# Optimization experiments

Hardware: AMD Instinct MI355X
Metric: run time of the kernel (lower is better)

The kernel has to match this reference:

```python
import jax, jax.numpy as jnp
import numpy as np

N = 100000       # nodes
E = 3200000      # edges
DIN = 128        # input_dim
H = 64           # hidden_dim
DEMB = 32        # embedding_dim
G = 256          # num graphs


def setup_inputs() -> dict:
    key = jax.random.key(0)
    ks = jax.random.split(key, 10)
    x = jax.random.normal(ks[0], (N, DIN), dtype=jnp.float32)
    edge_index = jax.random.randint(ks[1], (2, E), 0, N, dtype=jnp.int64)
    batch = jnp.sort(jax.random.randint(ks[2], (N,), 0, G, dtype=jnp.int64))
    W1 = jax.random.normal(ks[3], (DIN, H), dtype=jnp.float32) * (1.0 / np.sqrt(DIN))
    b1 = jnp.zeros((H,), dtype=jnp.float32)
    W2 = jax.random.normal(ks[4], (H, H), dtype=jnp.float32) * (1.0 / np.sqrt(H))
    b2 = jnp.zeros((H,), dtype=jnp.float32)
    Wl = jax.random.normal(ks[5], (H, DEMB), dtype=jnp.float32) * (1.0 / np.sqrt(H))
    bl = jnp.zeros((DEMB,), dtype=jnp.float32)
    return {"x": x, "edge_index": edge_index, "batch": batch, "num_graphs": G,
            "W1": W1, "b1": b1, "W2": W2, "b2": b2, "Wl": Wl, "bl": bl}


def _gcn_conv(h, src, dst, W, b, n_nodes):
    # PyG GCNConv: add self-loops, symmetric D^{-1/2}(A+I)D^{-1/2} normalization,
    # linear transform first, then propagate.
    h = h @ W                                                  # [N, out]
    deg = jax.ops.segment_sum(jnp.ones((src.shape[0],), h.dtype), dst,
                              num_segments=n_nodes) + 1.0      # +1 self-loop
    dinv = jax.lax.rsqrt(deg)                                  # [N]
    coef = dinv[src] * dinv[dst]                               # [E]
    msgs = h[src] * coef[:, None]                              # [E, out]
    agg = jax.ops.segment_sum(msgs, dst, num_segments=n_nodes)
    agg = agg + h * (dinv * dinv)[:, None]                     # self-loop message
    return agg + b


def reference(x, edge_index, batch, num_graphs, W1, b1, W2, b2, Wl, bl):
    src, dst = edge_index[0], edge_index[1]
    n_nodes = x.shape[0]
    h = jax.nn.relu(_gcn_conv(x, src, dst, W1, b1, n_nodes))
    h = jax.nn.relu(_gcn_conv(h, src, dst, W2, b2, n_nodes))
    # global_mean_pool over batch ids
    sums = jax.ops.segment_sum(h, batch, num_segments=num_graphs)     # [G, H]
    counts = jax.ops.segment_sum(jnp.ones((n_nodes,), h.dtype), batch,
                                 num_segments=num_graphs)
    pooled = sums / jnp.maximum(counts, 1.0)[:, None]
    return pooled @ Wl + bl                                           # [G, DEMB]
```

## Files before the change

### kernel.cpp

```cpp
#include <hip/hip_runtime.h>

#define NN 100000
#define NE 3200000
#define DIN 128
#define HD 64
#define DEMB 32
#define NG 256
#define NBUCK ((NN + 255) / 256)
#define NPB 512
#define CHUNK ((NE + NPB - 1) / NPB)
#define NM (NBUCK * NPB)
#define NMB ((NM + 1023) / 1024)

typedef unsigned short u16;
typedef unsigned int u32;

__device__ __forceinline__ float bflo(u32 u) { return __uint_as_float(u << 16); }
__device__ __forceinline__ float bfhi(u32 u) { return __uint_as_float(u & 0xffff0000u); }
__device__ __forceinline__ u16 f2bf(float f) {
    u32 u = __float_as_uint(f);
    return (u16)((u + 0x7fffu + ((u >> 16) & 1u)) >> 16);
}

__global__ __launch_bounds__(256) void k_blkhist(const int* __restrict__ dst,
                                                 int* __restrict__ HM, int E) {
    __shared__ int h[NBUCK];
    int blk = blockIdx.x, t = threadIdx.x;
    for (int i = t; i < NBUCK; i += 256) h[i] = 0;
    __syncthreads();
    int beg = blk * CHUNK, end = min(E, beg + CHUNK);
    for (int j = beg + t; j < end; j += 256) atomicAdd(&h[dst[j] >> 8], 1);
    __syncthreads();
    for (int i = t; i < NBUCK; i += 256) HM[i * NPB + blk] = h[i];
}

__global__ __launch_bounds__(1024) void k_scanA(int* __restrict__ HM,
                                                int* __restrict__ bsum, int n) {
    __shared__ int s[1024];
    int t = threadIdx.x;
    int idx = blockIdx.x * 1024 + t;
    int v = (idx < n) ? HM[idx] : 0;
    s[t] = v;
    __syncthreads();
    for (int off = 1; off < 1024; off <<= 1) {
        int add = (t >= off) ? s[t - off] : 0;
        __syncthreads();
        s[t] += add;
        __syncthreads();
    }
    if (idx < n) HM[idx] = s[t] - v;
    if (t == 1023) bsum[blockIdx.x] = s[t];
}

__global__ void k_scan2(const int* __restrict__ bsum, int* __restrict__ boff, int nb) {
    if (threadIdx.x == 0 && blockIdx.x == 0) {
        int acc = 0;
        for (int b = 0; b < nb; b++) { boff[b] = acc; acc += bsum[b]; }
        boff[nb] = acc;
    }
}

__global__ void k_scanC(int* __restrict__ HM, const int* __restrict__ boff, int n) {
    int idx = blockIdx.x * blockDim.x + threadIdx.x;
    if (idx < n) HM[idx] += boff[idx >> 10];
}

__global__ __launch_bounds__(256) void k_place(const int* __restrict__ src,
                                               const int* __restrict__ dst,
                                               const int* __restrict__ HM,
                                               int* __restrict__ part, int E) {
    __shared__ int cur[NBUCK];
    int blk = blockIdx.x, t = threadIdx.x;
    for (int i = t; i < NBUCK; i += 256) cur[i] = HM[i * NPB + blk];
    __syncthreads();
    int beg = blk * CHUNK, end = min(E, beg + CHUNK);
    for (int j = beg + t; j < end; j += 256) {
        int d = dst[j], s = src[j];
        int pos = atomicAdd(&cur[d >> 8], 1);
        part[pos] = s | ((d & 255) << 17);
    }
}

__global__ __launch_bounds__(256) void k_phaseB(const int* __restrict__ part,
                                                const int* __restrict__ HM,
                                                int* __restrict__ rowptr,
                                                int* __restrict__ ssrc,
                                                float* __restrict__ dinv, int E) {
    __shared__ int cnt[256];
    __shared__ int sc[256];
    int b = blockIdx.x;
    int t = threadIdx.x;
    int beg = HM[b * NPB];
    int end = (b == NBUCK - 1) ? E : HM[(b + 1) * NPB];
    int node0 = b << 8;
    int nnode = NN - node0 < 256 ? NN - node0 : 256;
    cnt[t] = 0;
    __syncthreads();
    for (int j = beg + t; j < end; j += 256) atomicAdd(&cnt[part[j] >> 17], 1);
    __syncthreads();
    int v = cnt[t];
    sc[t] = v;
    __syncthreads();
    for (int off = 1; off < 256; off <<= 1) {
        int add = (t >= off) ? sc[t - off] : 0;
        __syncthreads();
        sc[t] += add;
        __syncthreads();
    }
    int excl = sc[t] - v;
    if (t < nnode) {
        rowptr[node0 + t] = beg + excl;
        dinv[node0 + t] = rsqrtf((float)v + 1.0f);
    }
    if (b == NBUCK - 1 && t == 0) rowptr[NN] = E;
    __syncthreads();
    cnt[t] = beg + excl;
    __syncthreads();
    for (int j = beg + t; j < end; j += 256) {
        int e = part[j];
        int pos = atomicAdd(&cnt[e >> 17], 1);
        ssrc[pos] = e & 0x1FFFF;
    }
}

template <int K>
__global__ __launch_bounds__(256, 4) void k_gemm(const float* __restrict__ X,
                                                 const float* __restrict__ W,
                                                 const float* __restrict__ dinv,
                                                 u16* __restrict__ U, int n) {
    __shared__ __align__(16) float xt[32][68];
    __shared__ __align__(16) float wlc[32][64];
    int tid = threadIdx.x;
    int cg = tid & 15;
    int rs = tid >> 4;
    int row0 = blockIdx.x * 64;
    float4 acc0 = {0.f, 0.f, 0.f, 0.f};
    float4 acc1 = {0.f, 0.f, 0.f, 0.f};
    float4 acc2 = {0.f, 0.f, 0.f, 0.f};
    float4 acc3 = {0.f, 0.f, 0.f, 0.f};
    for (int kc = 0; kc < K; kc += 32) {
        __syncthreads();
        for (int p = 0; p < 2; ++p) {
            int idx = tid + p * 256;
            int r = idx >> 3;
            int c4 = idx & 7;
            int row = row0 + r;
            float4 v = {0.f, 0.f, 0.f, 0.f};
            if (row < n) v = *reinterpret_cast<const float4*>(&X[(size_t)row * K + kc + c4 * 4]);
            xt[c4 * 4 + 0][r] = v.x;
            xt[c4 * 4 + 1][r] = v.y;
            xt[c4 * 4 + 2][r] = v.z;
            xt[c4 * 4 + 3][r] = v.w;
        }
        for (int p = 0; p < 2; ++p) {
            int idx = tid + p * 256;
            int kr = idx >> 4;
            int c4 = idx & 15;
            *reinterpret_cast<float4*>(&wlc[kr][c4 * 4]) =
                *reinterpret_cast<const float4*>(&W[(size_t)(kc + kr) * 64 + c4 * 4]);
        }
        __syncthreads();
#pragma unroll
        for (int k = 0; k < 32; ++k) {
            float4 xv = *reinterpret_cast<const float4*>(&xt[k][rs * 4]);
            float4 wv = *reinterpret_cast<const float4*>(&wlc[k][cg * 4]);
            acc0.x += xv.x * wv.x; acc0.y += xv.x * wv.y; acc0.z += xv.x * wv.z; acc0.w += xv.x * wv.w;
            acc1.x += xv.y * wv.x; acc1.y += xv.y * wv.y; acc1.z += xv.y * wv.z; acc1.w += xv.y * wv.w;
            acc2.x += xv.z * wv.x; acc2.y += xv.z * wv.y; acc2.z += xv.z * wv.z; acc2.w += xv.z * wv.w;
            acc3.x += xv.w * wv.x; acc3.y += xv.w * wv.y; acc3.z += xv.w * wv.z; acc3.w += xv.w * wv.w;
        }
    }
    int rbase = row0 + rs * 4;
    float dv;
    if (rbase + 0 < n) { dv = dinv[rbase + 0];
        ushort4 o = {f2bf(acc0.x * dv), f2bf(acc0.y * dv), f2bf(acc0.z * dv), f2bf(acc0.w * dv)};
        *reinterpret_cast<ushort4*>(&U[(size_t)(rbase + 0) * 64 + cg * 4]) = o; }
    if (rbase + 1 < n) { dv = dinv[rbase + 1];
        ushort4 o = {f2bf(acc1.x * dv), f2bf(acc1.y * dv), f2bf(acc1.z * dv), f2bf(acc1.w * dv)};
        *reinterpret_cast<ushort4*>(&U[(size_t)(rbase + 1) * 64 + cg * 4]) = o; }
    if (rbase + 2 < n) { dv = dinv[rbase + 2];
        ushort4 o = {f2bf(acc2.x * dv), f2bf(acc2.y * dv), f2bf(acc2.z * dv), f2bf(acc2.w * dv)};
        *reinterpret_cast<ushort4*>(&U[(size_t)(rbase + 2) * 64 + cg * 4]) = o; }
    if (rbase + 3 < n) { dv = dinv[rbase + 3];
        ushort4 o = {f2bf(acc3.x * dv), f2bf(acc3.y * dv), f2bf(acc3.z * dv), f2bf(acc3.w * dv)};
        *reinterpret_cast<ushort4*>(&U[(size_t)(rbase + 3) * 64 + cg * 4]) = o; }
}

__global__ void k_gather(const int* __restrict__ rowptr, const int* __restrict__ ssrc,
                         const float* __restrict__ dinv, const u16* __restrict__ U,
                         const float* __restrict__ bias,
                         float* __restrict__ outbuf, int n) {
    int gtid = blockIdx.x * blockDim.x + threadIdx.x;
    int lane = gtid & 63;
    int g = lane & 7;
    int c = lane >> 3;
    int w = gtid >> 6;
    int nw = (gridDim.x * blockDim.x) >> 6;
    float bv = bias[lane];
    for (int d = w; d < n; d += nw) {
        int beg = rowptr[d], end = rowptr[d + 1];
        float4 aL0 = {0.f,0.f,0.f,0.f}, aH0 = {0.f,0.f,0.f,0.f};
        float4 aL1 = {0.f,0.f,0.f,0.f}, aH1 = {0.f,0.f,0.f,0.f};
        int j = beg;
        for (; j + 16 <= end; j += 16) {
            int s0 = ssrc[j + g];
            int s1 = ssrc[j + 8 + g];
            uint4 u0 = *reinterpret_cast<const uint4*>(&U[(size_t)s0 * 64 + c * 8]);
            uint4 u1 = *reinterpret_cast<const uint4*>(&U[(size_t)s1 * 64 + c * 8]);
            aL0.x += bflo(u0.x); aL0.y += bfhi(u0.x); aL0.z += bflo(u0.y); aL0.w += bfhi(u0.y);
            aH0.x += bflo(u0.z); aH0.y += bfhi(u0.z); aH0.z += bflo(u0.w); aH0.w += bfhi(u0.w);
            aL1.x += bflo(u1.x); aL1.y += bfhi(u1.x); aL1.z += bflo(u1.y); aL1.w += bfhi(u1.y);
            aH1.x += bflo(u1.z); aH1.y += bfhi(u1.z); aH1.z += bflo(u1.w); aH1.w += bfhi(u1.w);
        }
        if (j + 8 <= end) {
            int s0 = ssrc[j + g];
            uint4 u0 = *reinterpret_cast<const uint4*>(&U[(size_t)s0 * 64 + c * 8]);
            aL0.x += bflo(u0.x); aL0.y += bfhi(u0.x); aL0.z += bflo(u0.y); aL0.w += bfhi(u0.y);
            aH0.x += bflo(u0.z); aH0.y += bfhi(u0.z); aH0.z += bflo(u0.w); aH0.w += bfhi(u0.w);
            j += 8;
        }
        if (j + g < end) {
            int s1 = ssrc[j + g];
            uint4 u1 = *reinterpret_cast<const uint4*>(&U[(size_t)s1 * 64 + c * 8]);
            aL1.x += bflo(u1.x); aL1.y += bfhi(u1.x); aL1.z += bflo(u1.y); aL1.w += bfhi(u1.y);
            aH1.x += bflo(u1.z); aH1.y += bfhi(u1.z); aH1.z += bflo(u1.w); aH1.w += bfhi(u1.w);
        }
        aL0.x += aL1.x; aL0.y += aL1.y; aL0.z += aL1.z; aL0.w += aL1.w;
        aH0.x += aH1.x; aH0.y += aH1.y; aH0.z += aH1.z; aH0.w += aH1.w;
#pragma unroll
        for (int m = 1; m <= 4; m <<= 1) {
            aL0.x += __shfl_xor(aL0.x, m); aL0.y += __shfl_xor(aL0.y, m);
            aL0.z += __shfl_xor(aL0.z, m); aL0.w += __shfl_xor(aL0.w, m);
            aH0.x += __shfl_xor(aH0.x, m); aH0.y += __shfl_xor(aH0.y, m);
            aH0.z += __shfl_xor(aH0.z, m); aH0.w += __shfl_xor(aH0.w, m);
        }
        float4 q = (g & 4) ? aH0 : aL0;
        float hv = (g & 2) ? ((g & 1) ? q.w : q.z) : ((g & 1) ? q.y : q.x);
        float ud = bflo((u32)U[(size_t)d * 64 + lane] << 0) ;
        ud = __uint_as_float(((u32)U[(size_t)d * 64 + lane]) << 16);
        float dd = dinv[d];
        float h = (hv + ud) * dd + bv;
        h = h > 0.f ? h : 0.f;
        outbuf[(size_t)d * 64 + lane] = h;
    }
}

__global__ __launch_bounds__(256) void k_pool(const float* __restrict__ h,
                                              const int* __restrict__ batch,
                                              float* __restrict__ sums, int n) {
    int tid = blockIdx.x * blockDim.x + threadIdx.x;
    int wave = tid >> 6;
    int lane = tid & 63;
    int node0 = wave * 64;
    if (node0 >= n) return;
    int nodeEnd = min(n, node0 + 64);
    float acc = 0.f;
    int curg = batch[node0];
    for (int nd = node0; nd < nodeEnd; ++nd) {
        int g = batch[nd];
        if (g != curg) {
            atomicAdd(&sums[(size_t)curg * 64 + lane], acc);
            acc = 0.f;
            curg = g;
        }
        acc += h[(size_t)nd * 64 + lane];
    }
    atomicAdd(&sums[(size_t)curg * 64 + lane], acc);
}

__global__ void k_final(const float* __restrict__ sums, const int* __restrict__ batch,
                        const float* __restrict__ Wl, const float* __restrict__ bl,
                        float* __restrict__ out, int n) {
    __shared__ float pooled[64];
    int g = blockIdx.x;
    int t = threadIdx.x;
    int lo = 0, hi = n;
    while (lo < hi) { int m = (lo + hi) >> 1; if (batch[m] < g) lo = m + 1; else hi = m; }
    int lo2 = lo, hi2 = n;
    while (lo2 < hi2) { int m = (lo2 + hi2) >> 1; if (batch[m] < g + 1) lo2 = m + 1; else hi2 = m; }
    float c = (float)(lo2 - lo);
    c = c < 1.0f ? 1.0f : c;
    pooled[t] = sums[g * 64 + t] / c;
    __syncthreads();
    if (t < 32) {
        float acc = bl[t];
#pragma unroll 8
        for (int k = 0; k < 64; k++) acc += pooled[k] * Wl[k * 32 + t];
        out[g * 32 + t] = acc;
    }
}

extern "C" void kernel_launch(void* const* d_in, const int* in_sizes, int n_in,
                              void* d_out, int out_size, void* d_ws, size_t ws_size,
                              hipStream_t stream) {
    const float* x = (const float*)d_in[0];
    const int* ei = (const int*)d_in[1];
    const int* batch = (const int*)d_in[2];
    const float* W1 = (const float*)d_in[4];
    const float* b1 = (const float*)d_in[5];
    const float* W2 = (const float*)d_in[6];
    const float* b2 = (const float*)d_in[7];
    const float* Wl = (const float*)d_in[8];
    const float* bl = (const float*)d_in[9];
    float* out = (float*)d_out;

    const int* esrc = ei;
    const int* edst = ei + NE;

    char* ws = (char*)d_ws;
    size_t off = 0;
    auto alloc = [&](size_t bytes) {
        void* p = ws + off;
        off += (bytes + 255) & ~size_t(255);
        return p;
    };
    float* dinv   = (float*)alloc((size_t)NN * 4);
    int*   rowptr = (int*)alloc((size_t)(NN + 1) * 4);
    int*   HM     = (int*)alloc((size_t)NM * 4);
    int*   bsum   = (int*)alloc((size_t)(NMB + 1) * 4);
    int*   boff   = (int*)alloc((size_t)(NMB + 1) * 4);
    int*   ssrc   = (int*)alloc((size_t)NE * 4);
    u16*   tbuf   = (u16*)alloc((size_t)NE * 4);
    float* agg    = (float*)alloc((size_t)NN * HD * 4);
    float* sums   = (float*)alloc((size_t)NG * HD * 4);
    int* part = (int*)tbuf;

    k_blkhist<<<NPB, 256, 0, stream>>>(edst, HM, NE);
    k_scanA<<<NMB, 1024, 0, stream>>>(HM, bsum, NM);
    k_scan2<<<1, 64, 0, stream>>>(bsum, boff, NMB);
    k_scanC<<<(NM + 255) / 256, 256, 0, stream>>>(HM, boff, NM);
    k_place<<<NPB, 256, 0, stream>>>(esrc, edst, HM, part, NE);
    k_phaseB<<<NBUCK, 256, 0, stream>>>(part, HM, rowptr, ssrc, dinv, NE);

    k_gemm<DIN><<<(NN + 63) / 64, 256, 0, stream>>>(x, W1, dinv, tbuf, NN);
    k_gather<<<2048, 256, 0, stream>>>(rowptr, ssrc, dinv, tbuf, b1, agg, NN);

    k_gemm<HD><<<(NN + 63) / 64, 256, 0, stream>>>(agg, W2, dinv, tbuf, NN);
    k_gather<<<2048, 256, 0, stream>>>(rowptr, ssrc, dinv, tbuf, b2, agg, NN);

    hipMemsetAsync(sums, 0, (size_t)NG * HD * 4, stream);
    k_pool<<<(NN + 255) / 256, 256, 0, stream>>>(agg, batch, sums, NN);
    k_final<<<NG, 64, 0, stream>>>(sums, batch, Wl, bl, out, NN);
}
```

Measured before the change: 283.7 us.

## Fuse mean-pool into second gather and unroll edge loop to 32

The second aggregation kernel is templated to accumulate the pooled per-graph sums directly with segmented atomics, instead of writing the full node feature matrix and launching a separate pool kernel. Each wave now handles chunks of 16 consecutive nodes so runs of sorted batch ids can be reduced in registers before the atomic. The edge loop is unrolled to four independent 8-edge loads to raise memory-level parallelism. This removes one write and one read of the N×64 activation buffer and a launch. It costs coarser load balancing per wave and higher register pressure.

```diff
diff --git a/kernel.cpp b/kernel.cpp
--- a/kernel.cpp
+++ b/kernel.cpp
@@ -11,6 +11,7 @@
 #define CHUNK ((NE + NPB - 1) / NPB)
 #define NM (NBUCK * NPB)
 #define NMB ((NM + 1023) / 1024)
+#define GCH 16
 
 typedef unsigned short u16;
 typedef unsigned int u32;
@@ -186,9 +187,14 @@
         *reinterpret_cast<ushort4*>(&U[(size_t)(rbase + 3) * 64 + cg * 4]) = o; }
 }
 
+#define ACC8(u, L, H) \
+    L.x += bflo(u.x); L.y += bfhi(u.x); L.z += bflo(u.y); L.w += bfhi(u.y); \
+    H.x += bflo(u.z); H.y += bfhi(u.z); H.z += bflo(u.w); H.w += bfhi(u.w);
+
+template <bool FUSE_POOL>
 __global__ void k_gather(const int* __restrict__ rowptr, const int* __restrict__ ssrc,
                          const float* __restrict__ dinv, const u16* __restrict__ U,
-                         const float* __restrict__ bias,
+                         const float* __restrict__ bias, const int* __restrict__ batch,
                          float* __restrict__ outbuf, int n) {
     int gtid = blockIdx.x * blockDim.x + threadIdx.x;
     int lane = gtid & 63;
@@ -197,75 +203,85 @@
     int w = gtid >> 6;
     int nw = (gridDim.x * blockDim.x) >> 6;
     float bv = bias[lane];
-    for (int d = w; d < n; d += nw) {
-        int beg = rowptr[d], end = rowptr[d + 1];
-        float4 aL0 = {0.f,0.f,0.f,0.f}, aH0 = {0.f,0.f,0.f,0.f};
-        float4 aL1 = {0.f,0.f,0.f,0.f}, aH1 = {0.f,0.f,0.f,0.f};
-        int j = beg;
-        for (; j + 16 <= end; j += 16) {
-            int s0 = ssrc[j + g];
-            int s1 = ssrc[j + 8 + g];
-            uint4 u0 = *reinterpret_cast<const uint4*>(&U[(size_t)s0 * 64 + c * 8]);
-            uint4 u1 = *reinterpret_cast<const uint4*>(&U[(size_t)s1 * 64 + c * 8]);
-            aL0.x += bflo(u0.x); aL0.y += bfhi(u0.x); aL0.z += bflo(u0.y); aL0.w += bfhi(u0.y);
-            aH0.x += bflo(u0.z); aH0.y += bfhi(u0.z); aH0.z += bflo(u0.w); aH0.w += bfhi(u0.w);
-            aL1.x += bflo(u1.x); aL1.y += bfhi(u1.x); aL1.z += bflo(u1.y); aL1.w += bfhi(u1.y);
-            aH1.x += bflo(u1.z); aH1.y += bfhi(u1.z); aH1.z += bflo(u1.w); aH1.w += bfhi(u1.w);
+    int nch = (n + GCH - 1) / GCH;
+    for (int ch = w; ch < nch; ch += nw) {
+        int d0 = ch * GCH, d1 = min(n, d0 + GCH);
+        float pacc = 0.f;
+        int curg = FUSE_POOL ? batch[d0] : 0;
+        for (int d = d0; d < d1; ++d) {
+            int beg = rowptr[d], end = rowptr[d + 1];
+            float4 aL0 = {0.f,0.f,0.f,0.f}, aH0 = {0.f,0.f,0.f,0.f};
+            float4 aL1 = {0.f,0.f,0.f,0.f}, aH1 = {0.f,0.f,0.f,0.f};
+            float4 aL2 = {0.f,0.f,0.f,0.f}, aH2 = {0.f,0.f,0.f,0.f};
+            float4 aL3 = {0.f,0.f,0.f,0.f}, aH3 = {0.f,0.f,0.f,0.f};
+            int j = beg;
+            for (; j + 32 <= end; j += 32) {
+                int s0 = ssrc[j + g];
+                int s1 = ssrc[j + 8 + g];
+                int s2 = ssrc[j + 16 + g];
+                int s3 = ssrc[j + 24 + g];
+                uint4 u0 = *reinterpret_cast<const uint4*>(&U[(size_t)s0 * 64 + c * 8]);
+                uint4 u1 = *reinterpret_cast<const uint4*>(&U[(size_t)s1 * 64 + c * 8]);
+                uint4 u2 = *reinterpret_cast<const uint4*>(&U[(size_t)s2 * 64 + c * 8]);
+                uint4 u3 = *reinterpret_cast<const uint4*>(&U[(size_t)s3 * 64 + c * 8]);
+                ACC8(u0, aL0, aH0); ACC8(u1, aL1, aH1);
+                ACC8(u2, aL2, aH2); ACC8(u3, aL3, aH3);
+            }
+            if (j + 16 <= end) {
+                int s0 = ssrc[j + g];
+                int s1 = ssrc[j + 8 + g];
+                uint4 u0 = *reinterpret_cast<const uint4*>(&U[(size_t)s0 * 64 + c * 8]);
+                uint4 u1 = *reinterpret_cast<const uint4*>(&U[(size_t)s1 * 64 + c * 8]);
+                ACC8(u0, aL0, aH0); ACC8(u1, aL1, aH1);
+                j += 16;
+            }
+            if (j + 8 <= end) {
+                int s2 = ssrc[j + g];
+                uint4 u2 = *reinterpret_cast<const uint4*>(&U[(size_t)s2 * 64 + c * 8]);
+                ACC8(u2, aL2, aH2);
+                j += 8;
+            }
+            if (j + g < end) {
+                int s3 = ssrc[j + g];
+                uint4 u3 = *reinterpret_cast<const uint4*>(&U[(size_t)s3 * 64 + c * 8]);
+                ACC8(u3, aL3, aH3);
+            }
+            float4 aL, aH;
+            aL.x = (aL0.x + aL1.x) + (aL2.x + aL3.x);
+            aL.y = (aL0.y + aL1.y) + (aL2.y + aL3.y);
+            aL.z = (aL0.z + aL1.z) + (aL2.z + aL3.z);
+            aL.w = (aL0.w + aL1.w) + (aL2.w + aL3.w);
+            aH.x = (aH0.x + aH1.x) + (aH2.x + aH3.x);
+            aH.y = (aH0.y + aH1.y) + (aH2.y + aH3.y);
+            aH.z = (aH0.z + aH1.z) + (aH2.z + aH3.z);
+            aH.w = (aH0.w + aH1.w) + (aH2.w + aH3.w);
+#pragma unroll
+            for (int m = 1; m <= 4; m <<= 1) {
+                aL.x += __shfl_xor(aL.x, m); aL.y += __shfl_xor(aL.y, m);
+                aL.z += __shfl_xor(aL.z, m); aL.w += __shfl_xor(aL.w, m);
+                aH.x += __shfl_xor(aH.x, m); aH.y += __shfl_xor(aH.y, m);
+                aH.z += __shfl_xor(aH.z, m); aH.w += __shfl_xor(aH.w, m);
+            }
+            float4 q = (g & 4) ? aH : aL;
+            float hv = (g & 2) ? ((g & 1) ? q.w : q.z) : ((g & 1) ? q.y : q.x);
+            float ud = __uint_as_float(((u32)U[(size_t)d * 64 + lane]) << 16);
+            float dd = dinv[d];
+            float h = (hv + ud) * dd + bv;
+            h = h > 0.f ? h : 0.f;
+            if (FUSE_POOL) {
+                int gb = batch[d];
+                if (gb != curg) {
+                    atomicAdd(&outbuf[(size_t)curg * 64 + lane], pacc);
+                    pacc = 0.f;
+                    curg = gb;
+                }
+                pacc += h;
+            } else {
+                outbuf[(size_t)d * 64 + lane] = h;
+            }
         }
-        if (j + 8 <= end) {
-            int s0 = ssrc[j + g];
-            uint4 u0 = *reinterpret_cast<const uint4*>(&U[(size_t)s0 * 64 + c * 8]);
-            aL0.x += bflo(u0.x); aL0.y += bfhi(u0.x); aL0.z += bflo(u0.y); aL0.w += bfhi(u0.y);
-            aH0.x += bflo(u0.z); aH0.y += bfhi(u0.z); aH0.z += bflo(u0.w); aH0.w += bfhi(u0.w);
-            j += 8;
-        }
-        if (j + g < end) {
-            int s1 = ssrc[j + g];
-            uint4 u1 = *reinterpret_cast<const uint4*>(&U[(size_t)s1 * 64 + c * 8]);
-            aL1.x += bflo(u1.x); aL1.y += bfhi(u1.x); aL1.z += bflo(u1.y); aL1.w += bfhi(u1.y);
-            aH1.x += bflo(u1.z); aH1.y += bfhi(u1.z); aH1.z += bflo(u1.w); aH1.w += bfhi(u1.w);
-        }
-        aL0.x += aL1.x; aL0.y += aL1.y; aL0.z += aL1.z; aL0.w += aL1.w;
-        aH0.x += aH1.x; aH0.y += aH1.y; aH0.z += aH1.z; aH0.w += aH1.w;
-#pragma unroll
-        for (int m = 1; m <= 4; m <<= 1) {
-            aL0.x += __shfl_xor(aL0.x, m); aL0.y += __shfl_xor(aL0.y, m);
-            aL0.z += __shfl_xor(aL0.z, m); aL0.w += __shfl_xor(aL0.w, m);
-            aH0.x += __shfl_xor(aH0.x, m); aH0.y += __shfl_xor(aH0.y, m);
-            aH0.z += __shfl_xor(aH0.z, m); aH0.w += __shfl_xor(aH0.w, m);
-        }
-        float4 q = (g & 4) ? aH0 : aL0;
-        float hv = (g & 2) ? ((g & 1) ? q.w : q.z) : ((g & 1) ? q.y : q.x);
-        float ud = bflo((u32)U[(size_t)d * 64 + lane] << 0) ;
-        ud = __uint_as_float(((u32)U[(size_t)d * 64 + lane]) << 16);
-        float dd = dinv[d];
-        float h = (hv + ud) * dd + bv;
-        h = h > 0.f ? h : 0.f;
-        outbuf[(size_t)d * 64 + lane] = h;
-    }
-}
-
-__global__ __launch_bounds__(256) void k_pool(const float* __restrict__ h,
-                                              const int* __restrict__ batch,
-                                              float* __restrict__ sums, int n) {
-    int tid = blockIdx.x * blockDim.x + threadIdx.x;
-    int wave = tid >> 6;
-    int lane = tid & 63;
-    int node0 = wave * 64;
-    if (node0 >= n) return;
-    int nodeEnd = min(n, node0 + 64);
-    float acc = 0.f;
-    int curg = batch[node0];
-    for (int nd = node0; nd < nodeEnd; ++nd) {
-        int g = batch[nd];
-        if (g != curg) {
-            atomicAdd(&sums[(size_t)curg * 64 + lane], acc);
-            acc = 0.f;
-            curg = g;
-        }
-        acc += h[(size_t)nd * 64 + lane];
-    }
-    atomicAdd(&sums[(size_t)curg * 64 + lane], acc);
+        if (FUSE_POOL) atomicAdd(&outbuf[(size_t)curg * 64 + lane], pacc);
+    }
 }
 
 __global__ void k_final(const float* __restrict__ sums, const int* __restrict__ batch,
@@ -333,12 +349,11 @@
     k_phaseB<<<NBUCK, 256, 0, stream>>>(part, HM, rowptr, ssrc, dinv, NE);
 
     k_gemm<DIN><<<(NN + 63) / 64, 256, 0, stream>>>(x, W1, dinv, tbuf, NN);
-    k_gather<<<2048, 256, 0, stream>>>(rowptr, ssrc, dinv, tbuf, b1, agg, NN);
+    k_gather<false><<<2048, 256, 0, stream>>>(rowptr, ssrc, dinv, tbuf, b1, batch, agg, NN);
 
     k_gemm<HD><<<(NN + 63) / 64, 256, 0, stream>>>(agg, W2, dinv, tbuf, NN);
-    k_gather<<<2048, 256, 0, stream>>>(rowptr, ssrc, dinv, tbuf, b2, agg, NN);
-
     hipMemsetAsync(sums, 0, (size_t)NG * HD * 4, stream);
-    k_pool<<<(NN + 255) / 256, 256, 0, stream>>>(agg, batch, sums, NN);
+    k_gather<true><<<2048, 256, 0, stream>>>(rowptr, ssrc, dinv, tbuf, b2, batch, sums, NN);
+
     k_final<<<NG, 64, 0, stream>>>(sums, batch, Wl, bl, out, NN);
 }
```

New measurement: 336.6 us. 18.6% more time.
